# Optimization experiments

Measured on AMD Instinct MI355X. Metric: run time of the kernel, lower is better.

The kernel has to match this reference:

```python
import jax, jax.numpy as jnp
import numpy as np

N, E, D, H, DE, L, G = 50000, 800000, 64, 64, 16, 3, 512


def setup_inputs() -> dict:
    key = jax.random.key(0)
    ks = jax.random.split(key, 20)
    s = 0.05  # small init scale for numerical stability
    inp = {
        "x": jax.random.normal(ks[0], (N, D), dtype=jnp.float32),
        "edge_index": jax.random.randint(ks[1], (2, E), 0, N, dtype=jnp.int64),
        "edge_attr": jax.random.normal(ks[2], (E, DE), dtype=jnp.float32),
        "batch_idx": jnp.sort(jax.random.randint(ks[3], (N,), 0, G, dtype=jnp.int64)),
        "mW1": jax.random.normal(ks[4], (L, 2 * H + DE, H), dtype=jnp.float32) * s,
        "mb1": jnp.zeros((L, H), dtype=jnp.float32),
        "mW2": jax.random.normal(ks[5], (L, H, H), dtype=jnp.float32) * s,
        "mb2": jnp.zeros((L, H), dtype=jnp.float32),
        "uW1": jax.random.normal(ks[6], (L, 2 * H, H), dtype=jnp.float32) * s,
        "ub1": jnp.zeros((L, H), dtype=jnp.float32),
        "uW2": jax.random.normal(ks[7], (L, H, H), dtype=jnp.float32) * s,
        "ub2": jnp.zeros((L, H), dtype=jnp.float32),
        "lin1_w": jax.random.normal(ks[8], (H, H), dtype=jnp.float32) * s,
        "lin1_b": jnp.zeros((H,), dtype=jnp.float32),
        "lin2_w": jax.random.normal(ks[9], (H, 1), dtype=jnp.float32) * s,
        "lin2_b": jnp.zeros((1,), dtype=jnp.float32),
        "num_graphs": G,
    }
    return inp


def reference(x, edge_index, edge_attr, batch_idx, mW1, mb1, mW2, mb2,
              uW1, ub1, uW2, ub2, lin1_w, lin1_b, lin2_w, lin2_b, num_graphs):
    src = edge_index[0]  # x_j source nodes
    dst = edge_index[1]  # x_i target nodes (aggregation targets)
    n_nodes = x.shape[0]
    h = x
    for l in range(mW1.shape[0]):  # num_layers (small, fixed)
        # message: MLP(cat[x_i, x_j, edge_attr]) per edge -- [E, 2H+DE]
        m_in = jnp.concatenate([h[dst], h[src], edge_attr], axis=-1)
        m = jax.nn.relu(m_in @ mW1[l] + mb1[l]) @ mW2[l] + mb2[l]
        # aggregate: scatter-add messages into destination nodes -- [N, H]
        agg = jax.ops.segment_sum(m, dst, num_segments=n_nodes)
        # update: MLP(cat[x, aggr_out]), then outer ReLU from the model forward
        u_in = jnp.concatenate([h, agg], axis=-1)
        h = jax.nn.relu(jax.nn.relu(u_in @ uW1[l] + ub1[l]) @ uW2[l] + ub2[l])
    # global mean pool per graph -- [G, H]
    counts = jax.ops.segment_sum(jnp.ones((n_nodes,), h.dtype), batch_idx,
                                 num_segments=num_graphs)
    pooled = jax.ops.segment_sum(h, batch_idx, num_segments=num_graphs)
    pooled = pooled / jnp.maximum(counts, 1.0)[:, None]
    out = jax.nn.relu(pooled @ lin1_w + lin1_b) @ lin2_w + lin2_b  # [G, 1]
    return out
```

## Files before the change

### kernel.cpp

```cpp
#include <hip/hip_runtime.h>

#define H 64

typedef __attribute__((ext_vector_type(8))) short short8;
typedef __attribute__((ext_vector_type(4))) float floatx4;

__device__ __forceinline__ short bf16r(float f) {
    union { float f; unsigned u; } v; v.f = f;
    unsigned r = v.u + 0x7FFFu + ((v.u >> 16) & 1u);
    return (short)(r >> 16);
}

__device__ __forceinline__ void pack_one(const float* W, short* out, int K, int KT, int tid)
{
    const int lane = tid & 63;
    const int nt = (tid >> 6) & 3;
    const int lk = tid >> 8;
    const int kt = lk % KT;
    const int lay = lk / KT;
    const int n = nt * 16 + (lane & 15);
    const int kbase = kt * 32 + ((lane >> 4) & 3) * 8;
    short8 v;
#pragma unroll
    for (int j = 0; j < 8; ++j) {
        const int k = kbase + j;
        const float w = (k < K) ? W[((size_t)lay * K + k) * H + n] : 0.f;
        v[j] = bf16r(w);
    }
    *(short8*)(out + (size_t)tid * 8) = v;
}

#define T_MW1 3840
#define T_NW1 3072
#define T_UW2 1536

__global__ void prep_w2u(const float* __restrict__ mW2, const float* __restrict__ uW1,
                         const float* __restrict__ mb2,
                         float* __restrict__ nW1cat, float* __restrict__ c2u)
{
    int g = blockIdx.x * blockDim.x + threadIdx.x;
    if (g < 12288) {
        const int l = g >> 12, rem = g & 4095, a = rem >> 6, j = rem & 63;
        float s = 0.f;
#pragma unroll 8
        for (int c = 0; c < 64; ++c)
            s += mW2[((size_t)l * 64 + a) * 64 + c] * uW1[((size_t)l * 128 + 64 + c) * 64 + j];
        nW1cat[((size_t)l * 128 + 64 + a) * 64 + j] = s;
        return;
    }
    g -= 12288;
    if (g < 12288) {
        const int l = g >> 12, rem = g & 4095;
        nW1cat[(size_t)l * 8192 + rem] = uW1[(size_t)l * 8192 + rem];
        return;
    }
    g -= 12288;
    if (g < 192) {
        const int l = g >> 6, j = g & 63;
        float s = 0.f;
#pragma unroll 8
        for (int c = 0; c < 64; ++c)
            s += mb2[l * 64 + c] * uW1[((size_t)l * 128 + 64 + c) * 64 + j];
        c2u[l * 64 + j] = s;
    }
}

__global__ void prep_all(const float* __restrict__ mW1, const float* __restrict__ nW1cat,
                         const float* __restrict__ uW2, const float* __restrict__ x,
                         short* __restrict__ mW1f, short* __restrict__ nW1f,
                         short* __restrict__ uW2f, short* __restrict__ x16, int n8)
{
    int g = blockIdx.x * blockDim.x + threadIdx.x;
    if (g < T_MW1) { pack_one(mW1, mW1f, 144, 5, g); return; }
    g -= T_MW1;
    if (g < T_NW1) { pack_one(nW1cat, nW1f, 128, 4, g); return; }
    g -= T_NW1;
    if (g < T_UW2) { pack_one(uW2, uW2f, 64, 2, g); return; }
    g -= T_UW2;
    if (g < n8) {
        const float4 a = ((const float4*)x)[2 * g];
        const float4 b = ((const float4*)x)[2 * g + 1];
        short8 v;
        v[0] = bf16r(a.x); v[1] = bf16r(a.y); v[2] = bf16r(a.z); v[3] = bf16r(a.w);
        v[4] = bf16r(b.x); v[5] = bf16r(b.y); v[6] = bf16r(b.z); v[7] = bf16r(b.w);
        ((short8*)x16)[g] = v;
    }
}

__global__ void hist_kernel(const int* __restrict__ edst, int* __restrict__ cnt, int E)
{
    int e = blockIdx.x * blockDim.x + threadIdx.x;
    if (e < E) atomicAdd(&cnt[edst[e]], 1);
}

__global__ void scan_block(const int* __restrict__ cnt, int* __restrict__ offs,
                           int* __restrict__ bsum, int n)
{
    __shared__ int buf[1024];
    const int t = threadIdx.x;
    const int gid = blockIdx.x * 1024 + t;
    const int v = (gid < n) ? cnt[gid] : 0;
    buf[t] = v;
    __syncthreads();
#pragma unroll
    for (int off = 1; off < 1024; off <<= 1) {
        int x = (t >= off) ? buf[t - off] : 0;
        __syncthreads();
        buf[t] += x;
        __syncthreads();
    }
    if (gid < n) offs[gid] = buf[t] - v;
    if (t == 1023) bsum[blockIdx.x] = buf[1023];
}

__global__ void scan_bsum(int* __restrict__ bsum, int nb)
{
    if (threadIdx.x == 0) {
        int acc = 0;
        for (int i = 0; i < nb; ++i) { int v = bsum[i]; bsum[i] = acc; acc += v; }
    }
}

__global__ void add_bsum(int* __restrict__ offs, const int* __restrict__ bsum, int n)
{
    int gid = blockIdx.x * blockDim.x + threadIdx.x;
    if (gid < n) offs[gid] += bsum[gid >> 10];
}

__global__ void build_perm_gather(const int* __restrict__ esrc, const int* __restrict__ edst,
                                  const float* __restrict__ ea, int* __restrict__ offs,
                                  int* __restrict__ src_s, int* __restrict__ dst_s,
                                  short* __restrict__ ea16, int E)
{
    int e = blockIdx.x * blockDim.x + threadIdx.x;
    if (e >= E) return;
    const int d = edst[e];
    const int p = atomicAdd(&offs[d], 1);
    src_s[p] = esrc[e];
    dst_s[p] = d;
    const float4* r = (const float4*)(ea + (size_t)e * 16);
    const float4 a = r[0], b = r[1], c = r[2], d4 = r[3];
    short8 v0, v1;
    v0[0] = bf16r(a.x); v0[1] = bf16r(a.y); v0[2] = bf16r(a.z); v0[3] = bf16r(a.w);
    v0[4] = bf16r(b.x); v0[5] = bf16r(b.y); v0[6] = bf16r(b.z); v0[7] = bf16r(b.w);
    v1[0] = bf16r(c.x); v1[1] = bf16r(c.y); v1[2] = bf16r(c.z); v1[3] = bf16r(c.w);
    v1[4] = bf16r(d4.x); v1[5] = bf16r(d4.y); v1[6] = bf16r(d4.z); v1[7] = bf16r(d4.w);
    short8* o = (short8*)(ea16 + (size_t)p * 16);
    o[0] = v0; o[1] = v1;
}

__global__ __launch_bounds__(256, 5)
void pq_gemm(const short* __restrict__ h16, const short* __restrict__ W1fl,
             float* __restrict__ P32, float* __restrict__ Q32, int N)
{
    const int t = threadIdx.x;
    const int w = t >> 6, l = t & 63, q = l >> 4, m15 = l & 15;
    const int n0 = blockIdx.x * 64;
    const int n = n0 + w * 16 + m15;
    const bool ok = n < N;

    short8 a0 = {0,0,0,0,0,0,0,0}, a1 = a0;
    if (ok) {
        a0 = *(const short8*)(h16 + (size_t)n * H + q * 8);
        a1 = *(const short8*)(h16 + (size_t)n * H + 32 + q * 8);
    }

    floatx4 pa[4] = {{0,0,0,0},{0,0,0,0},{0,0,0,0},{0,0,0,0}};
    floatx4 qa[4] = {{0,0,0,0},{0,0,0,0},{0,0,0,0},{0,0,0,0}};
#pragma unroll
    for (int nt = 0; nt < 4; ++nt) {
        pa[nt] = __builtin_amdgcn_mfma_f32_16x16x32_bf16(a0, *(const short8*)(W1fl + ((0*4+nt)*64 + l)*8), pa[nt], 0,0,0);
        pa[nt] = __builtin_amdgcn_mfma_f32_16x16x32_bf16(a1, *(const short8*)(W1fl + ((1*4+nt)*64 + l)*8), pa[nt], 0,0,0);
        qa[nt] = __builtin_amdgcn_mfma_f32_16x16x32_bf16(a0, *(const short8*)(W1fl + ((2*4+nt)*64 + l)*8), qa[nt], 0,0,0);
        qa[nt] = __builtin_amdgcn_mfma_f32_16x16x32_bf16(a1, *(const short8*)(W1fl + ((3*4+nt)*64 + l)*8), qa[nt], 0,0,0);
    }
#pragma unroll
    for (int nt = 0; nt < 4; ++nt)
#pragma unroll
        for (int r = 0; r < 4; ++r) {
            const int nn = n0 + w * 16 + q * 4 + r;
            if (nn < N) {
                P32[(size_t)nn * H + nt * 16 + m15] = pa[nt][r];
                Q32[(size_t)nn * H + nt * 16 + m15] = qa[nt][r];
            }
        }
}

__global__ __launch_bounds__(256, 5)
void edge_msg_mfma(const float* __restrict__ P32, const float* __restrict__ Q32,
                   const int* __restrict__ src_s, const int* __restrict__ dst_s,
                   const short* __restrict__ ea16,
                   const short* __restrict__ W1cf, const float* __restrict__ b1,
                   float* __restrict__ aggH)
{
    __shared__ float smf[4 * 1056];
    const int t = threadIdx.x;
    const int w = t >> 6, l = t & 63, q = l >> 4, m15 = l & 15;
    const int i = blockIdx.x * 64 + w * 16 + m15;
    const int d = dst_s[i];
    const int s = src_s[i];
    float* C2 = smf + w * 1056;

    int dm[16], sm[16];
#pragma unroll
    for (int mm = 0; mm < 16; ++mm) {
        dm[mm] = __builtin_amdgcn_readlane(d, mm);
        sm[mm] = __builtin_amdgcn_readlane(s, mm);
    }
    float pv[16], qv[16];
#pragma unroll
    for (int mm = 0; mm < 16; ++mm) {
        pv[mm] = P32[(size_t)dm[mm] * H + l];
        qv[mm] = Q32[(size_t)sm[mm] * H + l];
    }
    const float b1l = b1[l];

    short8 a4 = {0, 0, 0, 0, 0, 0, 0, 0};
    if (q < 2) a4 = *(const short8*)(ea16 + (size_t)i * 16 + q * 8);

    floatx4 r4[4];
#pragma unroll
    for (int nt = 0; nt < 4; ++nt) {
        floatx4 z0 = {0, 0, 0, 0};
        r4[nt] = __builtin_amdgcn_mfma_f32_16x16x32_bf16(a4, *(const short8*)(W1cf + (nt*64 + l)*8), z0, 0,0,0);
    }
#pragma unroll
    for (int nt = 0; nt < 4; ++nt)
#pragma unroll
        for (int r = 0; r < 4; ++r)
            C2[(q * 4 + r) * 66 + nt * 16 + m15] = r4[nt][r];

    float run; int cur;
    {
        run = fmaxf(C2[l] + pv[0] + qv[0] + b1l, 0.f);
        cur = dm[0];
    }
#pragma unroll
    for (int mm = 1; mm < 16; ++mm) {
        const float val = fmaxf(C2[mm * 66 + l] + pv[mm] + qv[mm] + b1l, 0.f);
        if (dm[mm] != cur) {
            atomicAdd(&aggH[(size_t)cur * H + l], run);
            run = val; cur = dm[mm];
        } else {
            run += val;
        }
    }
    atomicAdd(&aggH[(size_t)cur * H + l], run);
}

__global__ __launch_bounds__(256, 5)
void node_update_mfma(const short* __restrict__ h16,
                      const float* __restrict__ aggH,
                      const short* __restrict__ W1f, const float* __restrict__ b1,
                      const short* __restrict__ W2f, const float* __restrict__ b2,
                      const float* __restrict__ c2u, const int* __restrict__ degc,
                      short* __restrict__ h16out,
                      const int* __restrict__ batch,
                      float* __restrict__ pooled, float* __restrict__ counts,
                      int N)
{
    __shared__ char smraw[16896];
    const int t = threadIdx.x;
    const int w = t >> 6, l = t & 63, q = l >> 4, m15 = l & 15;
    const int n0 = blockIdx.x * 64;
    const int n = n0 + w * 16 + m15;
    const bool ok = n < N;

    short* C1 = (short*)(smraw + w * 4224);
    float* C2 = (float*)(smraw + w * 4224);

    short8 a0 = {0,0,0,0,0,0,0,0}, a1 = a0, a2 = a0, a3 = a0;
    if (ok) {
        a0 = *(const short8*)(h16 + (size_t)n * H + q * 8);
        a1 = *(const short8*)(h16 + (size_t)n * H + 32 + q * 8);
        const float4 f0 = *(const float4*)(aggH + (size_t)n * H + q * 8);
        const float4 f1 = *(const float4*)(aggH + (size_t)n * H + q * 8 + 4);
        const float4 f2 = *(const float4*)(aggH + (size_t)n * H + 32 + q * 8);
        const float4 f3 = *(const float4*)(aggH + (size_t)n * H + 32 + q * 8 + 4);
        a2[0] = bf16r(f0.x); a2[1] = bf16r(f0.y); a2[2] = bf16r(f0.z); a2[3] = bf16r(f0.w);
        a2[4] = bf16r(f1.x); a2[5] = bf16r(f1.y); a2[6] = bf16r(f1.z); a2[7] = bf16r(f1.w);
        a3[0] = bf16r(f2.x); a3[1] = bf16r(f2.y); a3[2] = bf16r(f2.z); a3[3] = bf16r(f2.w);
        a3[4] = bf16r(f3.x); a3[5] = bf16r(f3.y); a3[6] = bf16r(f3.z); a3[7] = bf16r(f3.w);
    }

    float b1v[4], b2v[4], c2uv[4];
#pragma unroll
    for (int nt = 0; nt < 4; ++nt) {
        b1v[nt] = b1[nt * 16 + m15];
        b2v[nt] = b2[nt * 16 + m15];
        c2uv[nt] = c2u[nt * 16 + m15];
    }
    float degf[4];
#pragma unroll
    for (int r = 0; r < 4; ++r) {
        const int nn = n0 + w * 16 + q * 4 + r;
        degf[r] = (nn < N) ? (float)degc[nn] : 0.f;
    }

    floatx4 acc[4] = {{0,0,0,0},{0,0,0,0},{0,0,0,0},{0,0,0,0}};
#pragma unroll
    for (int nt = 0; nt < 4; ++nt) {
        acc[nt] = __builtin_amdgcn_mfma_f32_16x16x32_bf16(a0, *(const short8*)(W1f + ((0*4+nt)*64 + l)*8), acc[nt], 0,0,0);
        acc[nt] = __builtin_amdgcn_mfma_f32_16x16x32_bf16(a1, *(const short8*)(W1f + ((1*4+nt)*64 + l)*8), acc[nt], 0,0,0);
        acc[nt] = __builtin_amdgcn_mfma_f32_16x16x32_bf16(a2, *(const short8*)(W1f + ((2*4+nt)*64 + l)*8), acc[nt], 0,0,0);
        acc[nt] = __builtin_amdgcn_mfma_f32_16x16x32_bf16(a3, *(const short8*)(W1f + ((3*4+nt)*64 + l)*8), acc[nt], 0,0,0);
    }

#pragma unroll
    for (int nt = 0; nt < 4; ++nt)
#pragma unroll
        for (int r = 0; r < 4; ++r)
            C1[(q * 4 + r) * 72 + nt * 16 + m15] =
                bf16r(fmaxf(acc[nt][r] + b1v[nt] + degf[r] * c2uv[nt], 0.f));

    const short8 p0 = *(const short8*)(C1 + m15 * 72 + q * 8);
    const short8 p1 = *(const short8*)(C1 + m15 * 72 + 32 + q * 8);

    floatx4 c2[4] = {{0,0,0,0},{0,0,0,0},{0,0,0,0},{0,0,0,0}};
#pragma unroll
    for (int nt = 0; nt < 4; ++nt) {
        c2[nt] = __builtin_amdgcn_mfma_f32_16x16x32_bf16(p0, *(const short8*)(W2f + ((0*4+nt)*64 + l)*8), c2[nt], 0,0,0);
        c2[nt] = __builtin_amdgcn_mfma_f32_16x16x32_bf16(p1, *(const short8*)(W2f + ((1*4+nt)*64 + l)*8), c2[nt], 0,0,0);
    }

    if (!batch) {
#pragma unroll
        for (int nt = 0; nt < 4; ++nt)
#pragma unroll
            for (int r = 0; r < 4; ++r) {
                const int nn = n0 + w * 16 + q * 4 + r;
                if (nn < N)
                    h16out[(size_t)nn * H + nt * 16 + m15] =
                        bf16r(fmaxf(c2[nt][r] + b2v[nt], 0.f));
            }
        return;
    }

#pragma unroll
    for (int nt = 0; nt < 4; ++nt)
#pragma unroll
        for (int r = 0; r < 4; ++r)
            C2[(q * 4 + r) * 66 + nt * 16 + m15] = fmaxf(c2[nt][r] + b2v[nt], 0.f);

    const int bi = ok ? batch[n] : -1;
    int bm[16];
#pragma unroll
    for (int mm = 0; mm < 16; ++mm)
        bm[mm] = __builtin_amdgcn_readlane(bi, mm);
    float v[16];
#pragma unroll
    for (int mm = 0; mm < 16; ++mm) v[mm] = C2[mm * 66 + l];

    float run = v[0];
    int cur = bm[0];
    int len = 1;
#pragma unroll
    for (int mm = 1; mm < 16; ++mm) {
        if (bm[mm] != cur) {
            if (cur >= 0) {
                atomicAdd(&pooled[(size_t)cur * H + l], run);
                if (l == 0) atomicAdd(&counts[cur], (float)len);
            }
            run = v[mm]; cur = bm[mm]; len = 1;
        } else {
            run += v[mm]; ++len;
        }
    }
    if (cur >= 0) {
        atomicAdd(&pooled[(size_t)cur * H + l], run);
        if (l == 0) atomicAdd(&counts[cur], (float)len);
    }
}

__global__ void head_kernel(const float* __restrict__ pooled,
                            const float* __restrict__ counts,
                            const float* __restrict__ lin1w,
                            const float* __restrict__ lin1b,
                            const float* __restrict__ lin2w,
                            const float* __restrict__ lin2b,
                            float* __restrict__ out, int G)
{
    int g = blockIdx.x;
    int j = threadIdx.x;
    __shared__ float p[H];
    float c = fmaxf(counts[g], 1.0f);
    p[j] = pooled[(size_t)g * H + j] / c;
    __syncthreads();

    float accj = lin1b[j];
#pragma unroll
    for (int k = 0; k < H; ++k) accj = fmaf(p[k], lin1w[k * H + j], accj);
    accj = fmaxf(accj, 0.0f) * lin2w[j];
#pragma unroll
    for (int off = 32; off >= 1; off >>= 1) accj += __shfl_down(accj, off);
    if (j == 0) out[g] = accj + lin2b[0];
}

extern "C" void kernel_launch(void* const* d_in, const int* in_sizes, int n_in,
                              void* d_out, int out_size, void* d_ws, size_t ws_size,
                              hipStream_t stream)
{
    const float* x      = (const float*)d_in[0];
    const int*   eidx   = (const int*)d_in[1];
    const float* ea     = (const float*)d_in[2];
    const int*   batch  = (const int*)d_in[3];
    const float* mW1    = (const float*)d_in[4];
    const float* mb1    = (const float*)d_in[5];
    const float* mW2    = (const float*)d_in[6];
    const float* mb2    = (const float*)d_in[7];
    const float* uW1    = (const float*)d_in[8];
    const float* ub1    = (const float*)d_in[9];
    const float* uW2    = (const float*)d_in[10];
    const float* ub2    = (const float*)d_in[11];
    const float* lin1w  = (const float*)d_in[12];
    const float* lin1b  = (const float*)d_in[13];
    const float* lin2w  = (const float*)d_in[14];
    const float* lin2b  = (const float*)d_in[15];

    const int N = in_sizes[0] / H;
    const int E = in_sizes[1] / 2;
    const int G = out_size;

    short* mW1f = (short*)d_ws;
    short* nW1f = mW1f + 30720;
    short* uW2f = nW1f + 24576;
    short* x16  = uW2f + 12288;
    short* h16A = x16  + (size_t)N * H;
    short* h16B = h16A + (size_t)N * H;
    short* ea16 = h16B + (size_t)N * H;
    float* nW1cat = (float*)(ea16 + (size_t)E * 16);
    float* c2u    = nW1cat + 3 * 128 * 64;
    float* P32    = c2u + 192;
    float* Q32    = P32 + (size_t)N * H;
    char*  pch  = (char*)(Q32 + (size_t)N * H);
    int* offs   = (int*)pch;          pch += (size_t)N * 4;
    int* bsum   = (int*)pch;          pch += 256;
    int* src_s  = (int*)pch;          pch += (size_t)E * 4;
    int* dst_s  = (int*)pch;          pch += (size_t)E * 4;
    int*   cnt    = (int*)pch;
    float* agg3   = (float*)(pch + (size_t)N * 4);
    float* pooled = agg3 + (size_t)3 * N * H;
    float* counts = pooled + (size_t)G * H;
    const size_t zero_bytes = (size_t)N * 4 + ((size_t)3 * N * H + (size_t)G * H + G) * 4;

    const int* esrc = eidx;
    const int* edst = eidx + E;

    prep_w2u<<<(24768 + 255) / 256, 256, 0, stream>>>(mW2, uW1, mb2, nW1cat, c2u);
    {
        const int n8 = N * H / 8;
        const int total = T_MW1 + T_NW1 + T_UW2 + n8;
        prep_all<<<(total + 255) / 256, 256, 0, stream>>>(
            mW1, nW1cat, uW2, x, mW1f, nW1f, uW2f, x16, n8);
    }

    hipMemsetAsync(cnt, 0, zero_bytes, stream);

    hist_kernel<<<(E + 255) / 256, 256, 0, stream>>>(edst, cnt, E);
    {
        const int nb = (N + 1023) / 1024;
        scan_block<<<nb, 1024, 0, stream>>>(cnt, offs, bsum, N);
        scan_bsum<<<1, 64, 0, stream>>>(bsum, nb);
        add_bsum<<<(N + 255) / 256, 256, 0, stream>>>(offs, bsum, N);
    }
    build_perm_gather<<<(E + 255) / 256, 256, 0, stream>>>(
        esrc, edst, ea, offs, src_s, dst_s, ea16, E);

    const short* hin = x16;
    short* houts16[3] = {h16A, h16B, nullptr};
    const int nEB = E / 64;
    const int nNB = (N + 63) / 64;

    for (int lyr = 0; lyr < 3; ++lyr) {
        float* agg = agg3 + (size_t)lyr * N * H;
        pq_gemm<<<nNB, 256, 0, stream>>>(
            hin, mW1f + (size_t)lyr * 10240, P32, Q32, N);
        edge_msg_mfma<<<nEB, 256, 0, stream>>>(
            P32, Q32, src_s, dst_s, ea16,
            mW1f + (size_t)lyr * 10240 + 8192,
            mb1 + (size_t)lyr * H,
            agg);
        node_update_mfma<<<nNB, 256, 0, stream>>>(
            hin, agg,
            nW1f + (size_t)lyr * 8192, ub1 + (size_t)lyr * H,
            uW2f + (size_t)lyr * 4096, ub2 + (size_t)lyr * H,
            c2u + (size_t)lyr * 64, cnt,
            houts16[lyr],
            (lyr == 2) ? batch : (const int*)nullptr,
            pooled, counts, N);
        hin = houts16[lyr];
    }

    head_kernel<<<G, H, 0, stream>>>(pooled, counts, lin1w, lin1b, lin2w, lin2b,
                                     (float*)d_out, G);
}
```

Baseline: 402.2 us.

## Bucket edges by 64-node destination block and aggregate messages in LDS

Replaces the per-node CSR sort (histogram, three-kernel scan, perm) with a coarse sort into 64-node destination buckets, packing dst and src into one 32-bit word. A new per-bucket edge kernel computes the destination-side P projection on the fly into LDS, accumulates edge messages with LDS atomics, and writes aggregates and degree with plain stores. This removes global float atomics, the P32 buffer, and the big memset of the aggregation arrays. The packing assumes node ids fit in 16 bits, and heavily loaded buckets may become imbalanced.

```diff
diff --git a/kernel.cpp b/kernel.cpp
--- a/kernel.cpp
+++ b/kernel.cpp
@@ -87,19 +87,27 @@
     }
 }
 
-__global__ void hist_kernel(const int* __restrict__ edst, int* __restrict__ cnt, int E)
-{
-    int e = blockIdx.x * blockDim.x + threadIdx.x;
-    if (e < E) atomicAdd(&cnt[edst[e]], 1);
-}
-
-__global__ void scan_block(const int* __restrict__ cnt, int* __restrict__ offs,
-                           int* __restrict__ bsum, int n)
+__global__ void bucket_hist(const int* __restrict__ edst, int* __restrict__ bhist,
+                            int E, int nbk)
+{
+    __shared__ int lh[1024];
+    for (int i = threadIdx.x; i < nbk; i += 256) lh[i] = 0;
+    __syncthreads();
+    for (int e = blockIdx.x * 256 + threadIdx.x; e < E; e += gridDim.x * 256)
+        atomicAdd(&lh[edst[e] >> 6], 1);
+    __syncthreads();
+    for (int i = threadIdx.x; i < nbk; i += 256) {
+        const int v = lh[i];
+        if (v) atomicAdd(&bhist[i], v);
+    }
+}
+
+__global__ void bucket_scan(const int* __restrict__ bhist, int* __restrict__ bstart,
+                            int* __restrict__ bctr, int nbk, int E)
 {
     __shared__ int buf[1024];
     const int t = threadIdx.x;
-    const int gid = blockIdx.x * 1024 + t;
-    const int v = (gid < n) ? cnt[gid] : 0;
+    const int v = (t < nbk) ? bhist[t] : 0;
     buf[t] = v;
     __syncthreads();
 #pragma unroll
@@ -109,35 +117,20 @@
         buf[t] += x;
         __syncthreads();
     }
-    if (gid < n) offs[gid] = buf[t] - v;
-    if (t == 1023) bsum[blockIdx.x] = buf[1023];
-}
-
-__global__ void scan_bsum(int* __restrict__ bsum, int nb)
-{
-    if (threadIdx.x == 0) {
-        int acc = 0;
-        for (int i = 0; i < nb; ++i) { int v = bsum[i]; bsum[i] = acc; acc += v; }
-    }
-}
-
-__global__ void add_bsum(int* __restrict__ offs, const int* __restrict__ bsum, int n)
-{
-    int gid = blockIdx.x * blockDim.x + threadIdx.x;
-    if (gid < n) offs[gid] += bsum[gid >> 10];
-}
-
-__global__ void build_perm_gather(const int* __restrict__ esrc, const int* __restrict__ edst,
-                                  const float* __restrict__ ea, int* __restrict__ offs,
-                                  int* __restrict__ src_s, int* __restrict__ dst_s,
-                                  short* __restrict__ ea16, int E)
-{
-    int e = blockIdx.x * blockDim.x + threadIdx.x;
+    if (t < nbk) { const int ex = buf[t] - v; bstart[t] = ex; bctr[t] = ex; }
+    if (t == 0) bstart[nbk] = E;
+}
+
+__global__ void bucket_scatter(const int* __restrict__ esrc, const int* __restrict__ edst,
+                               const float* __restrict__ ea, int* __restrict__ bctr,
+                               unsigned* __restrict__ sd4, short* __restrict__ ea16s, int E)
+{
+    const int e = blockIdx.x * 256 + threadIdx.x;
     if (e >= E) return;
     const int d = edst[e];
-    const int p = atomicAdd(&offs[d], 1);
-    src_s[p] = esrc[e];
-    dst_s[p] = d;
+    const int s = esrc[e];
+    const int p = atomicAdd(&bctr[d >> 6], 1);
+    sd4[p] = ((unsigned)d << 16) | (unsigned)s;
     const float4* r = (const float4*)(ea + (size_t)e * 16);
     const float4 a = r[0], b = r[1], c = r[2], d4 = r[3];
     short8 v0, v1;
@@ -145,13 +138,13 @@
     v0[4] = bf16r(b.x); v0[5] = bf16r(b.y); v0[6] = bf16r(b.z); v0[7] = bf16r(b.w);
     v1[0] = bf16r(c.x); v1[1] = bf16r(c.y); v1[2] = bf16r(c.z); v1[3] = bf16r(c.w);
     v1[4] = bf16r(d4.x); v1[5] = bf16r(d4.y); v1[6] = bf16r(d4.z); v1[7] = bf16r(d4.w);
-    short8* o = (short8*)(ea16 + (size_t)p * 16);
+    short8* o = (short8*)(ea16s + (size_t)p * 16);
     o[0] = v0; o[1] = v1;
 }
 
 __global__ __launch_bounds__(256, 5)
-void pq_gemm(const short* __restrict__ h16, const short* __restrict__ W1fl,
-             float* __restrict__ P32, float* __restrict__ Q32, int N)
+void q_gemm(const short* __restrict__ h16, const short* __restrict__ W1fl,
+            float* __restrict__ Q32, int N)
 {
     const int t = threadIdx.x;
     const int w = t >> 6, l = t & 63, q = l >> 4, m15 = l & 15;
@@ -165,12 +158,9 @@
         a1 = *(const short8*)(h16 + (size_t)n * H + 32 + q * 8);
     }
 
-    floatx4 pa[4] = {{0,0,0,0},{0,0,0,0},{0,0,0,0},{0,0,0,0}};
     floatx4 qa[4] = {{0,0,0,0},{0,0,0,0},{0,0,0,0},{0,0,0,0}};
 #pragma unroll
     for (int nt = 0; nt < 4; ++nt) {
-        pa[nt] = __builtin_amdgcn_mfma_f32_16x16x32_bf16(a0, *(const short8*)(W1fl + ((0*4+nt)*64 + l)*8), pa[nt], 0,0,0);
-        pa[nt] = __builtin_amdgcn_mfma_f32_16x16x32_bf16(a1, *(const short8*)(W1fl + ((1*4+nt)*64 + l)*8), pa[nt], 0,0,0);
         qa[nt] = __builtin_amdgcn_mfma_f32_16x16x32_bf16(a0, *(const short8*)(W1fl + ((2*4+nt)*64 + l)*8), qa[nt], 0,0,0);
         qa[nt] = __builtin_amdgcn_mfma_f32_16x16x32_bf16(a1, *(const short8*)(W1fl + ((3*4+nt)*64 + l)*8), qa[nt], 0,0,0);
     }
@@ -179,73 +169,119 @@
 #pragma unroll
         for (int r = 0; r < 4; ++r) {
             const int nn = n0 + w * 16 + q * 4 + r;
-            if (nn < N) {
-                P32[(size_t)nn * H + nt * 16 + m15] = pa[nt][r];
-                Q32[(size_t)nn * H + nt * 16 + m15] = qa[nt][r];
-            }
-        }
-}
-
-__global__ __launch_bounds__(256, 5)
-void edge_msg_mfma(const float* __restrict__ P32, const float* __restrict__ Q32,
-                   const int* __restrict__ src_s, const int* __restrict__ dst_s,
-                   const short* __restrict__ ea16,
-                   const short* __restrict__ W1cf, const float* __restrict__ b1,
-                   float* __restrict__ aggH)
-{
-    __shared__ float smf[4 * 1056];
+            if (nn < N) Q32[(size_t)nn * H + nt * 16 + m15] = qa[nt][r];
+        }
+}
+
+__global__ __launch_bounds__(256, 4)
+void edge_bucket(const short* __restrict__ h16, const float* __restrict__ Q32,
+                 const unsigned* __restrict__ sd4, const short* __restrict__ ea16s,
+                 const int* __restrict__ bstart, const short* __restrict__ W1f,
+                 const float* __restrict__ b1,
+                 float* __restrict__ agg, float* __restrict__ degf, int N)
+{
+    __shared__ float ldsP[64 * 66];
+    __shared__ float ldsA[64 * 66];
+    __shared__ float ldsD[64];
     const int t = threadIdx.x;
     const int w = t >> 6, l = t & 63, q = l >> 4, m15 = l & 15;
-    const int i = blockIdx.x * 64 + w * 16 + m15;
-    const int d = dst_s[i];
-    const int s = src_s[i];
-    float* C2 = smf + w * 1056;
-
-    int dm[16], sm[16];
-#pragma unroll
-    for (int mm = 0; mm < 16; ++mm) {
-        dm[mm] = __builtin_amdgcn_readlane(d, mm);
-        sm[mm] = __builtin_amdgcn_readlane(s, mm);
-    }
-    float pv[16], qv[16];
-#pragma unroll
-    for (int mm = 0; mm < 16; ++mm) {
-        pv[mm] = P32[(size_t)dm[mm] * H + l];
-        qv[mm] = Q32[(size_t)sm[mm] * H + l];
-    }
-    const float b1l = b1[l];
-
-    short8 a4 = {0, 0, 0, 0, 0, 0, 0, 0};
-    if (q < 2) a4 = *(const short8*)(ea16 + (size_t)i * 16 + q * 8);
-
-    floatx4 r4[4];
+    const int nb0 = blockIdx.x << 6;
+    const int es = bstart[blockIdx.x], ee = bstart[blockIdx.x + 1];
+
+    {
+        const int n = nb0 + w * 16 + m15;
+        short8 a0 = {0,0,0,0,0,0,0,0}, a1 = a0;
+        if (n < N) {
+            a0 = *(const short8*)(h16 + (size_t)n * H + q * 8);
+            a1 = *(const short8*)(h16 + (size_t)n * H + 32 + q * 8);
+        }
+        floatx4 pa[4] = {{0,0,0,0},{0,0,0,0},{0,0,0,0},{0,0,0,0}};
+#pragma unroll
+        for (int nt = 0; nt < 4; ++nt) {
+            pa[nt] = __builtin_amdgcn_mfma_f32_16x16x32_bf16(a0, *(const short8*)(W1f + ((0*4+nt)*64 + l)*8), pa[nt], 0,0,0);
+            pa[nt] = __builtin_amdgcn_mfma_f32_16x16x32_bf16(a1, *(const short8*)(W1f + ((1*4+nt)*64 + l)*8), pa[nt], 0,0,0);
+        }
+#pragma unroll
+        for (int nt = 0; nt < 4; ++nt)
+#pragma unroll
+            for (int r = 0; r < 4; ++r)
+                ldsP[(w * 16 + q * 4 + r) * 66 + nt * 16 + m15] = pa[nt][r];
+    }
+    for (int i = t; i < 64 * 66; i += 256) ldsA[i] = 0.f;
+    if (t < 64) ldsD[t] = 0.f;
+    __syncthreads();
+
+    short8 wc[4];
+    float b1v[4];
 #pragma unroll
     for (int nt = 0; nt < 4; ++nt) {
-        floatx4 z0 = {0, 0, 0, 0};
-        r4[nt] = __builtin_amdgcn_mfma_f32_16x16x32_bf16(a4, *(const short8*)(W1cf + (nt*64 + l)*8), z0, 0,0,0);
-    }
-#pragma unroll
-    for (int nt = 0; nt < 4; ++nt)
-#pragma unroll
-        for (int r = 0; r < 4; ++r)
-            C2[(q * 4 + r) * 66 + nt * 16 + m15] = r4[nt][r];
-
-    float run; int cur;
+        wc[nt] = *(const short8*)(W1f + ((4*4 + nt) * 64 + l) * 8);
+        b1v[nt] = b1[nt * 16 + m15];
+    }
+
+    const int ntiles = (ee - es + 15) >> 4;
+    for (int ti = w; ti < ntiles; ti += 4) {
+        const int eb = es + ti * 16;
+        const int i  = eb + m15;
+
+        short8 a4 = {0,0,0,0,0,0,0,0};
+        if (q < 2) {
+            const int ic = (i < ee) ? i : (ee - 1);
+            a4 = *(const short8*)(ea16s + (size_t)ic * 16 + q * 8);
+        }
+        floatx4 acc[4];
+#pragma unroll
+        for (int nt = 0; nt < 4; ++nt) {
+            acc[nt][0] = b1v[nt]; acc[nt][1] = b1v[nt];
+            acc[nt][2] = b1v[nt]; acc[nt][3] = b1v[nt];
+        }
+#pragma unroll
+        for (int nt = 0; nt < 4; ++nt)
+            acc[nt] = __builtin_amdgcn_mfma_f32_16x16x32_bf16(a4, wc[nt], acc[nt], 0,0,0);
+
+        if (l < 16 && i < ee) {
+            const unsigned sdo = sd4[i];
+            atomicAdd(&ldsD[(sdo >> 16) & 63], 1.0f);
+        }
+
+#pragma unroll
+        for (int r = 0; r < 4; ++r) {
+            const int ei = eb + q * 4 + r;
+            const bool ok = ei < ee;
+            const unsigned sdv = sd4[ok ? ei : (ee - 1)];
+            const int drow = (sdv >> 16) & 63;
+            const int scol = sdv & 0xFFFF;
+            const float* qrow = Q32 + (size_t)scol * H + m15;
+#pragma unroll
+            for (int nt = 0; nt < 4; ++nt) {
+                const float pv = ldsP[drow * 66 + nt * 16 + m15];
+                const float qv = qrow[nt * 16];
+                float val = fmaxf(acc[nt][r] + pv + qv, 0.f);
+                if (!ok) val = 0.f;
+                atomicAdd(&ldsA[drow * 66 + nt * 16 + m15], val);
+            }
+        }
+    }
+    __syncthreads();
+
     {
-        run = fmaxf(C2[l] + pv[0] + qv[0] + b1l, 0.f);
-        cur = dm[0];
-    }
-#pragma unroll
-    for (int mm = 1; mm < 16; ++mm) {
-        const float val = fmaxf(C2[mm * 66 + l] + pv[mm] + qv[mm] + b1l, 0.f);
-        if (dm[mm] != cur) {
-            atomicAdd(&aggH[(size_t)cur * H + l], run);
-            run = val; cur = dm[mm];
-        } else {
-            run += val;
-        }
-    }
-    atomicAdd(&aggH[(size_t)cur * H + l], run);
+        const int row = t >> 2;
+        const int c0 = (t & 3) * 16;
+        const int n = nb0 + row;
+        if (n < N) {
+            float* dst = agg + (size_t)n * H + c0;
+#pragma unroll
+            for (int k = 0; k < 16; k += 4) {
+                float4 v;
+                v.x = ldsA[row * 66 + c0 + k];
+                v.y = ldsA[row * 66 + c0 + k + 1];
+                v.z = ldsA[row * 66 + c0 + k + 2];
+                v.w = ldsA[row * 66 + c0 + k + 3];
+                *(float4*)(dst + k) = v;
+            }
+        }
+        if (t < 64 && nb0 + t < N) degf[nb0 + t] = ldsD[t];
+    }
 }
 
 __global__ __launch_bounds__(256, 5)
@@ -253,7 +289,7 @@
                       const float* __restrict__ aggH,
                       const short* __restrict__ W1f, const float* __restrict__ b1,
                       const short* __restrict__ W2f, const float* __restrict__ b2,
-                      const float* __restrict__ c2u, const int* __restrict__ degc,
+                      const float* __restrict__ c2u, const float* __restrict__ degf,
                       short* __restrict__ h16out,
                       const int* __restrict__ batch,
                       float* __restrict__ pooled, float* __restrict__ counts,
@@ -290,11 +326,11 @@
         b2v[nt] = b2[nt * 16 + m15];
         c2uv[nt] = c2u[nt * 16 + m15];
     }
-    float degf[4];
+    float degv[4];
 #pragma unroll
     for (int r = 0; r < 4; ++r) {
         const int nn = n0 + w * 16 + q * 4 + r;
-        degf[r] = (nn < N) ? (float)degc[nn] : 0.f;
+        degv[r] = (nn < N) ? degf[nn] : 0.f;
     }
 
     floatx4 acc[4] = {{0,0,0,0},{0,0,0,0},{0,0,0,0},{0,0,0,0}};
@@ -311,7 +347,7 @@
 #pragma unroll
         for (int r = 0; r < 4; ++r)
             C1[(q * 4 + r) * 72 + nt * 16 + m15] =
-                bf16r(fmaxf(acc[nt][r] + b1v[nt] + degf[r] * c2uv[nt], 0.f));
+                bf16r(fmaxf(acc[nt][r] + b1v[nt] + degv[r] * c2uv[nt], 0.f));
 
     const short8 p0 = *(const short8*)(C1 + m15 * 72 + q * 8);
     const short8 p1 = *(const short8*)(C1 + m15 * 72 + 32 + q * 8);
@@ -420,6 +456,8 @@
     const int N = in_sizes[0] / H;
     const int E = in_sizes[1] / 2;
     const int G = out_size;
+    const int nbk = (N + 63) >> 6;
+    const int nbkp = (nbk + 3) & ~3;
 
     short* mW1f = (short*)d_ws;
     short* nW1f = mW1f + 30720;
@@ -427,21 +465,19 @@
     short* x16  = uW2f + 12288;
     short* h16A = x16  + (size_t)N * H;
     short* h16B = h16A + (size_t)N * H;
-    short* ea16 = h16B + (size_t)N * H;
-    float* nW1cat = (float*)(ea16 + (size_t)E * 16);
+    short* ea16s = h16B + (size_t)N * H;
+    unsigned* sd4 = (unsigned*)(ea16s + (size_t)E * 16);
+    float* nW1cat = (float*)(sd4 + (size_t)E);
     float* c2u    = nW1cat + 3 * 128 * 64;
-    float* P32    = c2u + 192;
-    float* Q32    = P32 + (size_t)N * H;
-    char*  pch  = (char*)(Q32 + (size_t)N * H);
-    int* offs   = (int*)pch;          pch += (size_t)N * 4;
-    int* bsum   = (int*)pch;          pch += 256;
-    int* src_s  = (int*)pch;          pch += (size_t)E * 4;
-    int* dst_s  = (int*)pch;          pch += (size_t)E * 4;
-    int*   cnt    = (int*)pch;
-    float* agg3   = (float*)(pch + (size_t)N * 4);
-    float* pooled = agg3 + (size_t)3 * N * H;
+    float* Q32    = c2u + 192;
+    float* degf   = Q32 + (size_t)N * H;
+    int* bstart   = (int*)(degf + N);
+    int* bctr     = bstart + nbkp + 4;
+    float* agg3   = (float*)(bctr + nbkp);
+    int*   bhist  = (int*)(agg3 + (size_t)3 * N * H);
+    float* pooled = (float*)(bhist + nbkp);
     float* counts = pooled + (size_t)G * H;
-    const size_t zero_bytes = (size_t)N * 4 + ((size_t)3 * N * H + (size_t)G * H + G) * 4;
+    const size_t zero_bytes = (size_t)nbkp * 4 + ((size_t)G * H + G) * 4;
 
     const int* esrc = eidx;
     const int* edst = eidx + E;
@@ -454,37 +490,30 @@
             mW1, nW1cat, uW2, x, mW1f, nW1f, uW2f, x16, n8);
     }
 
-    hipMemsetAsync(cnt, 0, zero_bytes, stream);
-
-    hist_kernel<<<(E + 255) / 256, 256, 0, stream>>>(edst, cnt, E);
-    {
-        const int nb = (N + 1023) / 1024;
-        scan_block<<<nb, 1024, 0, stream>>>(cnt, offs, bsum, N);
-        scan_bsum<<<1, 64, 0, stream>>>(bsum, nb);
-        add_bsum<<<(N + 255) / 256, 256, 0, stream>>>(offs, bsum, N);
-    }
-    build_perm_gather<<<(E + 255) / 256, 256, 0, stream>>>(
-        esrc, edst, ea, offs, src_s, dst_s, ea16, E);
+    hipMemsetAsync(bhist, 0, zero_bytes, stream);
+
+    bucket_hist<<<256, 256, 0, stream>>>(edst, bhist, E, nbk);
+    bucket_scan<<<1, 1024, 0, stream>>>(bhist, bstart, bctr, nbk, E);
+    bucket_scatter<<<(E + 255) / 256, 256, 0, stream>>>(
+        esrc, edst, ea, bctr, sd4, ea16s, E);
 
     const short* hin = x16;
     short* houts16[3] = {h16A, h16B, nullptr};
-    const int nEB = E / 64;
     const int nNB = (N + 63) / 64;
 
     for (int lyr = 0; lyr < 3; ++lyr) {
         float* agg = agg3 + (size_t)lyr * N * H;
-        pq_gemm<<<nNB, 256, 0, stream>>>(
-            hin, mW1f + (size_t)lyr * 10240, P32, Q32, N);
-        edge_msg_mfma<<<nEB, 256, 0, stream>>>(
-            P32, Q32, src_s, dst_s, ea16,
-            mW1f + (size_t)lyr * 10240 + 8192,
-            mb1 + (size_t)lyr * H,
-            agg);
+        q_gemm<<<nNB, 256, 0, stream>>>(
+            hin, mW1f + (size_t)lyr * 10240, Q32, N);
+        edge_bucket<<<nbk, 256, 0, stream>>>(
+            hin, Q32, sd4, ea16s, bstart,
+            mW1f + (size_t)lyr * 10240, mb1 + (size_t)lyr * H,
+            agg, degf, N);
         node_update_mfma<<<nNB, 256, 0, stream>>>(
             hin, agg,
             nW1f + (size_t)lyr * 8192, ub1 + (size_t)lyr * H,
             uW2f + (size_t)lyr * 4096, ub2 + (size_t)lyr * H,
-            c2u + (size_t)lyr * 64, cnt,
+            c2u + (size_t)lyr * 64, degf,
             houts16[lyr],
             (lyr == 2) ? batch : (const int*)nullptr,
             pooled, counts, N);
```

Measured after the change: 1.463 ms. 3.64x slower.
